# Kernel tuning notes

Hardware: AMD Instinct MI355X
Metric: run time of the kernel (lower is better)

## Reference

```python
import jax, jax.numpy as jnp
import numpy as np

# Wrapped module: Linear(2048->8192) + ReLU + Linear(8192->2048), both with bias.
D_IN, D_FF, D_OUT = 2048, 8192, 2048
N_W1 = D_FF * D_IN
N_B1 = D_FF
N_W2 = D_OUT * D_FF
N_B2 = D_OUT
NUM_WANDB = N_W1 + N_B1 + N_W2 + N_B2  # 33,564,672
SIZE_N = 5794  # ceil(sqrt(NUM_WANDB))
SIZE_M = 2897  # ceil(1.0 * SIZE_N / 2)
BATCH = 4096


def setup_inputs() -> dict:
    key = jax.random.key(0)
    k1, k2, k3 = jax.random.split(key, 3)
    x = jax.random.normal(k1, (BATCH, D_IN), dtype=jnp.float32)
    # scale factors keep reconstructed weights in a sane numeric range
    V1 = jax.random.normal(k2, (SIZE_N, SIZE_M), dtype=jnp.float32) * 0.02
    V2 = jax.random.normal(k3, (SIZE_N, SIZE_M), dtype=jnp.float32) * 0.02
    return {"x": x, "V1": V1, "V2": V2}


def reference(x, V1, V2):
    # V = V1 @ V2^T, flattened row-major (matches torch .view(-1, 1))
    V = jnp.matmul(V1, V2.T).reshape(-1)
    # Vectorized equivalent of WandBtoV's per-element copy loop:
    # consecutive slices of V fill each weight/bias in named_modules order.
    o = 0
    W1 = V[o:o + N_W1].reshape(D_FF, D_IN); o += N_W1   # linear1.weight [out,in]
    b1 = V[o:o + N_B1]; o += N_B1                        # linear1.bias
    W2 = V[o:o + N_W2].reshape(D_OUT, D_FF); o += N_W2   # linear2.weight
    b2 = V[o:o + N_B2]                                   # linear2.bias
    h = jax.nn.relu(jnp.matmul(x, W1.T) + b1)            # [B, D_FF]
    return jnp.matmul(h, W2.T) + b2                      # [B, D_OUT]
```

## Files before the change

### kernel.cpp

```cpp
#include <hip/hip_runtime.h>
#include <hip/hip_bf16.h>

typedef __attribute__((ext_vector_type(8))) __bf16 bf16x8;
typedef __attribute__((ext_vector_type(4))) __bf16 bf16x4;
typedef __attribute__((ext_vector_type(16))) float f32x16;

#define D_IN   2048
#define D_FF   8192
#define D_OUT  2048
#define BATCH  4096
#define SIZE_N 5794
#define SIZE_M 2897
#define PN 5888
#define PK 2944

#define OFF_B1 16777216
#define OFF_W2 16785408
#define OFF_B2 33562624

#define BM 128
#define BN 128
#define BK 64

__device__ __forceinline__ void gload_lds16(const __bf16* g, __bf16* lds) {
    __builtin_amdgcn_global_load_lds(
        (const __attribute__((address_space(1))) void*)g,
        (__attribute__((address_space(3))) void*)lds,
        16, 0, 0);
}

template<int MODE>
__global__ __launch_bounds__(256)
void gemm_nt(const __bf16* __restrict__ A, int lda,
             const __bf16* __restrict__ B, int ldb,
             void* __restrict__ Cv, int ldc,
             const __bf16* __restrict__ bias,
             int K, int Mvalid, int Nvalid)
{
    __shared__ bf16x8 As[BM * 8];
    __shared__ bf16x8 Bs[BN * 8];

    const int tid  = threadIdx.x;
    const int wave = tid >> 6;
    const int lane = tid & 63;

    const int bm0 = blockIdx.x * BM;
    const int bn0 = blockIdx.y * BN;

    const int wm = (wave >> 1) * 64;
    const int wn = (wave & 1) * 64;

    const int srow8 = lane >> 3;
    const int sc8   = ((lane & 7) ^ srow8) * 8;

    const __bf16* aptr = A + (size_t)(bm0 + wave * 32 + srow8) * lda + sc8;
    const __bf16* bptr = B + (size_t)(bn0 + wave * 32 + srow8) * ldb + sc8;

    const int fr  = lane & 31;
    const int kh  = lane >> 5;
    const int frs = fr & 7;
    const int aRow0 = (wm + fr) * 8;
    const int aRow1 = (wm + 32 + fr) * 8;
    const int bRow0 = (wn + fr) * 8;
    const int bRow1 = (wn + 32 + fr) * 8;

    f32x16 acc[2][2] = {};

    const int kTiles = K / BK;
    for (int kt = 0; kt < kTiles; ++kt) {
        #pragma unroll
        for (int i = 0; i < 4; ++i) {
            gload_lds16(aptr + (size_t)(8 * i) * lda,
                        (__bf16*)&As[(wave * 32 + 8 * i) * 8]);
            gload_lds16(bptr + (size_t)(8 * i) * ldb,
                        (__bf16*)&Bs[(wave * 32 + 8 * i) * 8]);
        }
        aptr += BK;
        bptr += BK;
        __builtin_amdgcn_s_waitcnt(0);
        __syncthreads();

        #pragma unroll
        for (int w = 0; w < 4; ++w) {
            const int sl = (2 * w + kh) ^ frs;
            bf16x8 a0 = As[aRow0 + sl];
            bf16x8 a1 = As[aRow1 + sl];
            bf16x8 b0 = Bs[bRow0 + sl];
            bf16x8 b1 = Bs[bRow1 + sl];
            acc[0][0] = __builtin_amdgcn_mfma_f32_32x32x16_bf16(a0, b0, acc[0][0], 0, 0, 0);
            acc[0][1] = __builtin_amdgcn_mfma_f32_32x32x16_bf16(a0, b1, acc[0][1], 0, 0, 0);
            acc[1][0] = __builtin_amdgcn_mfma_f32_32x32x16_bf16(a1, b0, acc[1][0], 0, 0, 0);
            acc[1][1] = __builtin_amdgcn_mfma_f32_32x32x16_bf16(a1, b1, acc[1][1], 0, 0, 0);
        }

        __syncthreads();
    }

    const int ecol  = lane & 31;
    const int erow0 = 4 * kh;
    #pragma unroll
    for (int i = 0; i < 2; ++i) {
        #pragma unroll
        for (int j = 0; j < 2; ++j) {
            const int colBase = bn0 + wn + j * 32 + ecol;
            #pragma unroll
            for (int reg = 0; reg < 16; ++reg) {
                const int row = bm0 + wm + i * 32 + (reg & 3) + 8 * (reg >> 2) + erow0;
                float v = acc[i][j][reg];
                if constexpr (MODE == 0) {
                    if (row < Mvalid && colBase < Nvalid)
                        ((__bf16*)Cv)[(size_t)row * ldc + colBase] = (__bf16)v;
                } else if constexpr (MODE == 1) {
                    v += (float)bias[colBase];
                    v = v > 0.f ? v : 0.f;
                    ((__bf16*)Cv)[(size_t)row * ldc + colBase] = (__bf16)v;
                } else {
                    v += (float)bias[colBase];
                    ((float*)Cv)[(size_t)row * ldc + colBase] = v;
                }
            }
        }
    }
}

__global__ void pad_cvt_bf16(const float* __restrict__ in, __bf16* __restrict__ out,
                             int rows, int cols, int pcols, int total)
{
    int idx = blockIdx.x * blockDim.x + threadIdx.x;
    if (idx >= total) return;
    int r = idx / pcols;
    int c = idx - r * pcols;
    float v = (r < rows && c < cols) ? in[(size_t)r * cols + c] : 0.0f;
    out[idx] = (__bf16)v;
}

__global__ void cvt_bf16_vec(const float4* __restrict__ in, bf16x4* __restrict__ out, int n4)
{
    int i = blockIdx.x * blockDim.x + threadIdx.x;
    if (i >= n4) return;
    float4 v = in[i];
    bf16x4 o;
    o.x = (__bf16)v.x; o.y = (__bf16)v.y; o.z = (__bf16)v.z; o.w = (__bf16)v.w;
    out[i] = o;
}

extern "C" void kernel_launch(void* const* d_in, const int* in_sizes, int n_in,
                              void* d_out, int out_size, void* d_ws, size_t ws_size,
                              hipStream_t stream)
{
    const float* x  = (const float*)d_in[0];
    const float* V1 = (const float*)d_in[1];
    const float* V2 = (const float*)d_in[2];
    float* out = (float*)d_out;

    char* ws = (char*)d_ws;
    const size_t vbElems  = (size_t)SIZE_N * SIZE_N;
    const size_t padElems = (size_t)PN * PK;

    size_t off = 0;
    __bf16* Vb = (__bf16*)(ws + off);
    off += ((vbElems * 2 + 255) / 256) * 256;
    __bf16* V1b = (__bf16*)(ws + off);
    __bf16* V2b = V1b + padElems;
    __bf16* hb  = (__bf16*)(ws + off);
    off += ((2 * padElems * 2 + 255) / 256) * 256;
    __bf16* xb = (__bf16*)(ws + off);
    off += (size_t)BATCH * D_IN * 2;
    if (ws_size < off) return;

    {
        int total  = (int)padElems;
        int blocks = (total + 255) / 256;
        pad_cvt_bf16<<<blocks, 256, 0, stream>>>(V1, V1b, SIZE_N, SIZE_M, PK, total);
        pad_cvt_bf16<<<blocks, 256, 0, stream>>>(V2, V2b, SIZE_N, SIZE_M, PK, total);
        int n4 = BATCH * D_IN / 4;
        cvt_bf16_vec<<<(n4 + 255) / 256, 256, 0, stream>>>((const float4*)x, (bf16x4*)xb, n4);
    }

    gemm_nt<0><<<dim3(PN / BM, PN / BN), 256, 0, stream>>>(
        V1b, PK, V2b, PK, (void*)Vb, SIZE_N, (const __bf16*)nullptr, PK, SIZE_N, SIZE_N);

    gemm_nt<1><<<dim3(BATCH / BM, D_FF / BN), 256, 0, stream>>>(
        xb, D_IN, Vb, D_IN, (void*)hb, D_FF, Vb + OFF_B1, D_IN, BATCH, D_FF);

    gemm_nt<2><<<dim3(BATCH / BM, D_OUT / BN), 256, 0, stream>>>(
        hb, D_FF, Vb + OFF_W2, D_FF, (void*)out, D_OUT, Vb + OFF_B2, D_FF, BATCH, D_OUT);
}
```

Before: 740.9 us.

## Rewrite GEMM with 4-stage LDS pipeline, larger 512-thread tiles, and priority hints

Replaces the single-buffered 128x128x64 GEMM with a templated kernel that uses 256x256 (or 128x256) tiles across 8 waves. It prefetches three K-tiles ahead into a 4-deep LDS ring buffer, using explicit vmcnt waits instead of full waitcnt plus double syncthreads. MFMA blocks are wrapped in setprio. The aim is to hide global-load latency and raise arithmetic intensity per block, at the cost of larger LDS use and more register pressure. The grid for PN=5888 with 256 tiles is 23x23, which may leave CUs underused.

Measured after the change: 780.0 us. 1.05x slower.

```diff
diff --git a/kernel.cpp b/kernel.cpp
--- a/kernel.cpp
+++ b/kernel.cpp
@@ -18,9 +18,8 @@
 #define OFF_W2 16785408
 #define OFF_B2 33562624
 
-#define BM 128
-#define BN 128
-#define BK 64
+#define BK   32
+#define NBUF 4
 
 __device__ __forceinline__ void gload_lds16(const __bf16* g, __bf16* lds) {
     __builtin_amdgcn_global_load_lds(
@@ -29,16 +28,34 @@
         16, 0, 0);
 }
 
-template<int MODE>
-__global__ __launch_bounds__(256)
-void gemm_nt(const __bf16* __restrict__ A, int lda,
-             const __bf16* __restrict__ B, int ldb,
-             void* __restrict__ Cv, int ldc,
-             const __bf16* __restrict__ bias,
-             int K, int Mvalid, int Nvalid)
-{
-    __shared__ bf16x8 As[BM * 8];
-    __shared__ bf16x8 Bs[BN * 8];
+template<int N> __device__ __forceinline__ void wait_vmcnt() {
+    static_assert(N == 0 || N == 3 || N == 4 || N == 6 || N == 8, "unsupported vmcnt");
+    if constexpr (N == 0)      asm volatile("s_waitcnt vmcnt(0)" ::: "memory");
+    else if constexpr (N == 3) asm volatile("s_waitcnt vmcnt(3)" ::: "memory");
+    else if constexpr (N == 4) asm volatile("s_waitcnt vmcnt(4)" ::: "memory");
+    else if constexpr (N == 6) asm volatile("s_waitcnt vmcnt(6)" ::: "memory");
+    else                       asm volatile("s_waitcnt vmcnt(8)" ::: "memory");
+}
+__device__ __forceinline__ void wait_lgkm0() {
+    asm volatile("s_waitcnt lgkmcnt(0)" ::: "memory");
+}
+
+template<int MODE, int BM, int BN>
+__global__ __launch_bounds__(512, 2)
+void gemm_nt2(const __bf16* __restrict__ A, int lda,
+              const __bf16* __restrict__ B, int ldb,
+              void* __restrict__ Cv, int ldc,
+              const __bf16* __restrict__ bias,
+              int K, int Mvalid, int Nvalid)
+{
+    constexpr int LA = BM / 128;
+    constexpr int LB = BN / 128;
+    constexpr int L  = LA + LB;
+    constexpr int FM = BM / 64;
+    constexpr int FN = BN / 128;
+    constexpr int ROWS = BM + BN;
+
+    __shared__ bf16x8 lds[NBUF * ROWS * 4];
 
     const int tid  = threadIdx.x;
     const int wave = tid >> 6;
@@ -47,66 +64,91 @@
     const int bm0 = blockIdx.x * BM;
     const int bn0 = blockIdx.y * BN;
 
-    const int wm = (wave >> 1) * 64;
-    const int wn = (wave & 1) * 64;
-
-    const int srow8 = lane >> 3;
-    const int sc8   = ((lane & 7) ^ srow8) * 8;
-
-    const __bf16* aptr = A + (size_t)(bm0 + wave * 32 + srow8) * lda + sc8;
-    const __bf16* bptr = B + (size_t)(bn0 + wave * 32 + srow8) * ldb + sc8;
+    const int wm = wave >> 2;
+    const int wn = wave & 3;
+
+    const int srow   = lane >> 2;
+    const int schunk = ((lane & 3) ^ ((lane >> 3) & 3)) * 8;
+
+    const __bf16* aS = A + (size_t)(bm0 + wave * (BM / 8) + srow) * lda + schunk;
+    const __bf16* bS = B + (size_t)(bn0 + wave * (BN / 8) + srow) * ldb + schunk;
+
+    auto stage = [&](int t) {
+        const int bb = t & (NBUF - 1);
+        bf16x8* bufA = &lds[bb * ROWS * 4];
+        bf16x8* bufB = bufA + BM * 4;
+        const size_t kof = (size_t)t * BK;
+        #pragma unroll
+        for (int i = 0; i < LA; ++i)
+            gload_lds16(aS + kof + (size_t)(16 * i) * lda,
+                        (__bf16*)&bufA[(wave * (BM / 8) + 16 * i) * 4]);
+        #pragma unroll
+        for (int i = 0; i < LB; ++i)
+            gload_lds16(bS + kof + (size_t)(16 * i) * ldb,
+                        (__bf16*)&bufB[(wave * (BN / 8) + 16 * i) * 4]);
+    };
 
     const int fr  = lane & 31;
     const int kh  = lane >> 5;
-    const int frs = fr & 7;
-    const int aRow0 = (wm + fr) * 8;
-    const int aRow1 = (wm + 32 + fr) * 8;
-    const int bRow0 = (wn + fr) * 8;
-    const int bRow1 = (wn + 32 + fr) * 8;
-
-    f32x16 acc[2][2] = {};
-
-    const int kTiles = K / BK;
-    for (int kt = 0; kt < kTiles; ++kt) {
-        #pragma unroll
-        for (int i = 0; i < 4; ++i) {
-            gload_lds16(aptr + (size_t)(8 * i) * lda,
-                        (__bf16*)&As[(wave * 32 + 8 * i) * 8]);
-            gload_lds16(bptr + (size_t)(8 * i) * ldb,
-                        (__bf16*)&Bs[(wave * 32 + 8 * i) * 8]);
+    const int swz = (fr >> 1) & 3;
+
+    f32x16 acc[FM][FN] = {};
+
+    const int nt = K / BK;
+
+    stage(0); stage(1); stage(2);
+    wait_vmcnt<2 * L>();
+    __builtin_amdgcn_s_barrier();
+
+    for (int t = 0; t < nt; ++t) {
+        if (t + 3 < nt) stage(t + 3);
+
+        const int bb = t & (NBUF - 1);
+        const bf16x8* bufA = &lds[bb * ROWS * 4];
+        const bf16x8* bufB = bufA + BM * 4;
+
+        #pragma unroll
+        for (int ks = 0; ks < 2; ++ks) {
+            const int sl = (2 * ks + kh) ^ swz;
+            bf16x8 af[FM], bq[FN];
+            #pragma unroll
+            for (int m = 0; m < FM; ++m)
+                af[m] = bufA[(wm * (BM / 2) + m * 32 + fr) * 4 + sl];
+            #pragma unroll
+            for (int n = 0; n < FN; ++n)
+                bq[n] = bufB[(wn * (BN / 4) + n * 32 + fr) * 4 + sl];
+            __builtin_amdgcn_s_setprio(1);
+            #pragma unroll
+            for (int m = 0; m < FM; ++m) {
+                #pragma unroll
+                for (int n = 0; n < FN; ++n)
+                    acc[m][n] = __builtin_amdgcn_mfma_f32_32x32x16_bf16(
+                        af[m], bq[n], acc[m][n], 0, 0, 0);
+            }
+            __builtin_amdgcn_s_setprio(0);
         }
-        aptr += BK;
-        bptr += BK;
-        __builtin_amdgcn_s_waitcnt(0);
-        __syncthreads();
-
-        #pragma unroll
-        for (int w = 0; w < 4; ++w) {
-            const int sl = (2 * w + kh) ^ frs;
-            bf16x8 a0 = As[aRow0 + sl];
-            bf16x8 a1 = As[aRow1 + sl];
-            bf16x8 b0 = Bs[bRow0 + sl];
-            bf16x8 b1 = Bs[bRow1 + sl];
-            acc[0][0] = __builtin_amdgcn_mfma_f32_32x32x16_bf16(a0, b0, acc[0][0], 0, 0, 0);
-            acc[0][1] = __builtin_amdgcn_mfma_f32_32x32x16_bf16(a0, b1, acc[0][1], 0, 0, 0);
-            acc[1][0] = __builtin_amdgcn_mfma_f32_32x32x16_bf16(a1, b0, acc[1][0], 0, 0, 0);
-            acc[1][1] = __builtin_amdgcn_mfma_f32_32x32x16_bf16(a1, b1, acc[1][1], 0, 0, 0);
+
+        if (t + 1 < nt) {
+            wait_lgkm0();
+            if      (t + 3 < nt) wait_vmcnt<2 * L>();
+            else if (t + 2 < nt) wait_vmcnt<L>();
+            else                 wait_vmcnt<0>();
+            __builtin_amdgcn_s_barrier();
         }
-
-        __syncthreads();
     }
 
-    const int ecol  = lane & 31;
-    const int erow0 = 4 * kh;
+    const int ecol = lane & 31;
+    const int er0  = 4 * kh;
     #pragma unroll
-    for (int i = 0; i < 2; ++i) {
-        #pragma unroll
-        for (int j = 0; j < 2; ++j) {
-            const int colBase = bn0 + wn + j * 32 + ecol;
+    for (int m = 0; m < FM; ++m) {
+        #pragma unroll
+        for (int n = 0; n < FN; ++n) {
+            const int colBase = bn0 + wn * (BN / 4) + n * 32 + ecol;
             #pragma unroll
             for (int reg = 0; reg < 16; ++reg) {
-                const int row = bm0 + wm + i * 32 + (reg & 3) + 8 * (reg >> 2) + erow0;
-                float v = acc[i][j][reg];
+                const int row = bm0 + wm * (BM / 2) + m * 32
+                              + (reg & 3) + 8 * (reg >> 2) + er0;
+                float v = acc[m][n][reg];
                 if constexpr (MODE == 0) {
                     if (row < Mvalid && colBase < Nvalid)
                         ((__bf16*)Cv)[(size_t)row * ldc + colBase] = (__bf16)v;
@@ -177,12 +219,12 @@
         cvt_bf16_vec<<<(n4 + 255) / 256, 256, 0, stream>>>((const float4*)x, (bf16x4*)xb, n4);
     }
 
-    gemm_nt<0><<<dim3(PN / BM, PN / BN), 256, 0, stream>>>(
+    gemm_nt2<0, 256, 256><<<dim3(PN / 256, PN / 256), 512, 0, stream>>>(
         V1b, PK, V2b, PK, (void*)Vb, SIZE_N, (const __bf16*)nullptr, PK, SIZE_N, SIZE_N);
 
-    gemm_nt<1><<<dim3(BATCH / BM, D_FF / BN), 256, 0, stream>>>(
+    gemm_nt2<1, 256, 256><<<dim3(BATCH / 256, D_FF / 256), 512, 0, stream>>>(
         xb, D_IN, Vb, D_IN, (void*)hb, D_FF, Vb + OFF_B1, D_IN, BATCH, D_FF);
 
-    gemm_nt<2><<<dim3(BATCH / BM, D_OUT / BN), 256, 0, stream>>>(
+    gemm_nt2<2, 128, 256><<<dim3(BATCH / 128, D_OUT / 256), 512, 0, stream>>>(
         hb, D_FF, Vb + OFF_W2, D_FF, (void*)out, D_OUT, Vb + OFF_B2, D_FF, BATCH, D_OUT);
 }
```
